# Performance work log

Measured on AMD Instinct MI355X. Metric: run time of the kernel, lower is better.

## Reference

```python
import jax, jax.numpy as jnp
import numpy as np

N_NODES, N_EDGES, N_REL, F_DIM, N_HEAD, N_LAYERS = 20000, 100000, 1000, 128, 4, 4
NEG_SLOPE = 0.2  # PyG GATv2Conv default negative_slope


def _gatv2_layer(x, ea_full, src, dst, Wl, bl, Wr, br, We, att, bias):
    # x: [N, F]; ea_full: [Etot, F] edge attrs (incl. self-loop rows)
    N = x.shape[0]
    H, C = att.shape  # heads, out-dim per head
    xl = (x @ Wl + bl).reshape(N, H, C)          # source-side projection
    xr = (x @ Wr + br).reshape(N, H, C)          # target-side projection
    ee = (ea_full @ We).reshape(-1, H, C)        # [Etot, H, C] edge embedding
    # GATv2 scoring: leaky_relu(x_i + x_j + e) . att
    e = jax.nn.leaky_relu(xl[src] + xr[dst] + ee, NEG_SLOPE)
    logits = jnp.einsum('ehc,hc->eh', e, att)    # [Etot, H]
    # segment softmax over edges grouped by destination node
    m = jax.ops.segment_max(logits, dst, num_segments=N)
    p = jnp.exp(logits - m[dst])
    denom = jax.ops.segment_sum(p, dst, num_segments=N)
    alpha = p / denom[dst]                       # [Etot, H]
    out = jax.ops.segment_sum(alpha[:, :, None] * xl[src], dst, num_segments=N)
    return out.mean(axis=1) + bias               # concat=False -> head mean


def setup_inputs() -> dict:
    key = jax.random.key(0)
    ks = jax.random.split(key, 12)
    N, E, R, F, H, L = N_NODES, N_EDGES, N_REL, F_DIM, N_HEAD, N_LAYERS
    HC = H * F
    s = 1.0 / np.sqrt(F)
    return {
        'x': jax.random.normal(ks[0], (N, F), jnp.float32),
        'edge_index': jax.random.randint(ks[1], (2, E), 0, N, dtype=jnp.int32),
        'relations': jax.random.normal(ks[2], (R, F), jnp.float32),
        'relation_index': jax.random.randint(ks[3], (E,), 0, R, dtype=jnp.int32),
        'Wl': jax.random.normal(ks[4], (L, F, HC), jnp.float32) * s,
        'bl': jnp.zeros((L, HC), jnp.float32),
        'Wr': jax.random.normal(ks[5], (L, F, HC), jnp.float32) * s,
        'br': jnp.zeros((L, HC), jnp.float32),
        'We': jax.random.normal(ks[6], (L, F, HC), jnp.float32) * s,
        'att': jax.random.normal(ks[7], (L, H, F), jnp.float32) * s,
        'bias': jnp.zeros((L, F), jnp.float32),
    }


def reference(x, edge_index, relations, relation_index, Wl, bl, Wr, br, We, att, bias):
    N = x.shape[0]
    sl = jnp.arange(N, dtype=edge_index.dtype)
    src = jnp.concatenate([edge_index[0], sl])   # add_self_loops=True
    dst = jnp.concatenate([edge_index[1], sl])
    ea = relations[relation_index]               # [E, F]
    # self-loop edge_attr uses fill_value='mean' (PyG default)
    ea_mean = ea.mean(axis=0)
    ea_full = jnp.concatenate([ea, jnp.broadcast_to(ea_mean, (N, ea.shape[1]))])
    h = x
    for l in range(N_LAYERS):
        h = _gatv2_layer(h, ea_full, src, dst, Wl[l], bl[l], Wr[l], br[l], We[l], att[l], bias[l])
    return (h, relations)
```

## Files before the change

kernel.cpp:

```cpp
#include <hip/hip_runtime.h>
#include <hip/hip_bf16.h>

#define N_NODES   20000
#define N_EDGES   100000
#define N_REL     1000
#define F_DIM     128
#define N_HEAD    4
#define HC        512
#define HC2       256
#define N_LAYERS  4
#define REL_EXT_ROWS 1008
#define NEG_SLOPE 0.2f
#define NODE_MB   ((N_NODES + 63) / 64)
#define REL_MB    ((REL_EXT_ROWS + 63) / 64)

typedef __attribute__((ext_vector_type(8))) short short8;
typedef __attribute__((ext_vector_type(4))) float floatx4;

__device__ __forceinline__ float loadIn(const void* p, size_t i, int f32) {
    if (f32) return ((const float*)p)[i];
    union { unsigned int u; float f; } c;
    c.u = ((unsigned int)((const unsigned short*)p)[i]) << 16;
    return c.f;
}

__device__ __forceinline__ unsigned short f2bf(float v) {
    __hip_bfloat16 b = __float2bfloat16(v);
    return *(unsigned short*)&b;
}

__device__ __forceinline__ void unpack2(unsigned int u, float& lo, float& hi) {
    union { unsigned int u; float f; } a, b;
    a.u = u << 16;
    b.u = u & 0xFFFF0000u;
    lo = a.f; hi = b.f;
}

__global__ void detect_kernel(const unsigned short* __restrict__ x, int* __restrict__ flag) {
    int t = threadIdx.x;
    int cnt = 0;
    for (int j = t; j < 256; j += 64) {
        int e = (x[j] >> 7) & 0xFF;
        if (e >= 143) cnt++;
    }
    for (int off = 32; off; off >>= 1) cnt += __shfl_xor(cnt, off);
    if (t == 0) flag[0] = (cnt >= 8) ? 1 : 0;
}


__global__ void hist_kernel(const int* __restrict__ dst, const int* __restrict__ rel,
                            int* __restrict__ deg, int* __restrict__ rcount) {
    int e = blockIdx.x * 256 + threadIdx.x;
    if (e < N_EDGES) {
        atomicAdd(&deg[dst[e]], 1);
        atomicAdd(&rcount[rel[e]], 1);
    }
}

__global__ void ea_mean_kernel(const int* __restrict__ rcount,
                               const void* __restrict__ relations,
                               float* __restrict__ ea_mean, const int* __restrict__ flag) {
    int f32 = flag[0];
    int b = blockIdx.x;
    int t = threadIdx.x;
    int col = t & 127;
    int rhalf = t >> 7;
    float acc = 0.f;
    for (int j = 0; j < 4; ++j) {
        int r = b * 8 + j * 2 + rhalf;
        acc += (float)rcount[r] * loadIn(relations, (size_t)r * F_DIM + col, f32);
    }
    __shared__ float part[256];
    part[t] = acc;
    __syncthreads();
    if (t < 128)
        atomicAdd(&ea_mean[col], (part[t] + part[t + 128]) * (1.f / (float)N_EDGES));
}

__global__ void relext_kernel(const void* __restrict__ relations,
                              const float* __restrict__ ea_mean,
                              unsigned short* __restrict__ rel_ext, const int* __restrict__ flag) {
    int idx = blockIdx.x * 256 + threadIdx.x;
    if (idx >= REL_EXT_ROWS * F_DIM) return;
    int f32 = flag[0];
    int r = idx >> 7;
    int c = idx & 127;
    float v;
    if (r < N_REL)       v = loadIn(relations, idx, f32);
    else if (r == N_REL) v = ea_mean[c];
    else                 v = 0.f;
    rel_ext[idx] = f2bf(v);
}

__global__ void scan_kernel(const int* __restrict__ deg,
                            int* __restrict__ row_start, int* __restrict__ cursor) {
    __shared__ int part[1024];
    int t = threadIdx.x;
    const int CH = (N_NODES + 1023) / 1024;
    int base = t * CH;
    int sum = 0;
    for (int j = 0; j < CH; ++j) {
        int idx = base + j;
        if (idx < N_NODES) sum += deg[idx];
    }
    part[t] = sum;
    __syncthreads();
    for (int off = 1; off < 1024; off <<= 1) {
        int u = (t >= off) ? part[t - off] : 0;
        __syncthreads();
        part[t] += u;
        __syncthreads();
    }
    int run = part[t] - sum;
    for (int j = 0; j < CH; ++j) {
        int idx = base + j;
        if (idx < N_NODES) {
            row_start[idx] = run;
            cursor[idx] = run;
            run += deg[idx];
        }
    }
    if (t == 1023) row_start[N_NODES] = part[1023];
}

__global__ void scatter_kernel(const int* __restrict__ src, const int* __restrict__ dst,
                               const int* __restrict__ rel, int* __restrict__ cursor,
                               int* __restrict__ csr_pack) {
    int e = blockIdx.x * 256 + threadIdx.x;
    if (e < N_EDGES) {
        int d = dst[e];
        int p = atomicAdd(&cursor[d], 1);
        csr_pack[p] = src[e] | (rel[e] << 16);
    }
}

__global__ void tail_kernel(const void* __restrict__ relations, void* __restrict__ out,
                            const int* __restrict__ flag) {
    int i = blockIdx.x * 256 + threadIdx.x;
    if (i >= N_REL * F_DIM) return;
    int f32 = flag[0];
    float v = loadIn(relations, i, f32);
    size_t o = (size_t)N_NODES * F_DIM + i;
    if (f32) ((float*)out)[o] = v;
    else     ((unsigned short*)out)[o] = f2bf(v);
}

__global__ void w_transpose_kernel(const void* __restrict__ Wl, const void* __restrict__ Wr,
                                   const void* __restrict__ We,
                                   unsigned short* __restrict__ Wt, const int* __restrict__ flag) {
    int f32 = flag[0];
    int k0 = blockIdx.x * 64;
    int n0 = blockIdx.y * 64;
    int mat = blockIdx.z;
    const void* src = (mat < 4) ? Wl : (mat < 8 ? Wr : We);
    size_t base = (size_t)(mat & 3) * F_DIM * HC;
    unsigned short* dst = Wt + (size_t)mat * HC * F_DIM;
    __shared__ float T[64][65];
    int t = threadIdx.x;
    int r = t >> 2, cq = t & 3;
    for (int j = 0; j < 16; ++j) {
        int n = cq * 16 + j;
        T[n][r] = loadIn(src, base + (size_t)(k0 + r) * HC + n0 + n, f32);
    }
    __syncthreads();
    for (int j = 0; j < 16; ++j) {
        int k = cq * 16 + j;
        dst[(size_t)(n0 + r) * F_DIM + k0 + k] = f2bf(T[r][k]);
    }
}

__launch_bounds__(256, 4)
__global__ void proj_kernel(const void* __restrict__ A_node, int a_input,
                            const unsigned short* __restrict__ rel_ext,
                            const unsigned short* __restrict__ Wlt,
                            const unsigned short* __restrict__ Wrt,
                            const unsigned short* __restrict__ Wet,
                            const void* __restrict__ bl, const void* __restrict__ br,
                            size_t boff,
                            unsigned short* __restrict__ xl,
                            unsigned short* __restrict__ xr,
                            unsigned short* __restrict__ re,
                            const int* __restrict__ flag) {
    __shared__ __align__(16) short As[64][136];
    __shared__ __align__(16) short BtRaw[128 * 72];
    int f32 = flag[0];
    int isNode = (blockIdx.x < NODE_MB);
    int m0 = (isNode ? blockIdx.x : (blockIdx.x - NODE_MB)) * 64;
    int M = isNode ? N_NODES : REL_EXT_ROWS;
    int tpb = isNode ? 2 : 1;
    int a_f32 = (isNode && a_input) ? f32 : 0;
    const void* A = isNode ? A_node : (const void*)rel_ext;
    int t = threadIdx.x;

    for (int j = 0; j < 4; ++j) {
        int c = t + j * 256;
        int row = c >> 4;
        int colc = (c & 15) * 8;
        int gm = m0 + row;
        short8 v = (short8){0, 0, 0, 0, 0, 0, 0, 0};
        if (gm < M) {
            size_t idx = (size_t)gm * F_DIM + colc;
            if (a_f32) {
                const float* Af = (const float*)A;
                for (int q = 0; q < 8; ++q) v[q] = (short)f2bf(Af[idx + q]);
            } else {
                v = *(const short8*)((const unsigned short*)A + idx);
            }
        }
        *(short8*)&As[row][colc] = v;
    }

    int wave = t >> 6, lane = t & 63;
    int wm = (wave >> 1) * 32, wn = (wave & 1) * 64;
    int r16 = lane & 15, quad = lane >> 4;

    for (int it = 0; it < tpb; ++it) {
        int nt = isNode ? (blockIdx.y * 2 + it) : blockIdx.y;
        const unsigned short* Wt = isNode ? ((nt < 4) ? Wlt : Wrt) : Wet;
        int n0 = (nt & 3) * 128;

        floatx4 acc[2][4];
        for (int mi = 0; mi < 2; ++mi)
            for (int ni = 0; ni < 4; ++ni)
                acc[mi][ni] = (floatx4){0.f, 0.f, 0.f, 0.f};

        for (int half = 0; half < 2; ++half) {
            __syncthreads();
            for (int j = 0; j < 4; ++j) {
                int c = t + j * 256;
                int nl = c >> 3;
                int kc = (c & 7) * 8;
                *(short8*)&BtRaw[nl * 72 + kc] =
                    *(const short8*)(Wt + (size_t)(n0 + nl) * F_DIM + half * 64 + kc);
            }
            __syncthreads();

            for (int kk = 0; kk < 2; ++kk) {
                short8 a[2], b[4];
                for (int mi = 0; mi < 2; ++mi)
                    a[mi] = *(const short8*)&As[wm + mi * 16 + r16][half * 64 + kk * 32 + quad * 8];
                for (int ni = 0; ni < 4; ++ni)
                    b[ni] = *(const short8*)&BtRaw[(wn + ni * 16 + r16) * 72 + kk * 32 + quad * 8];
                for (int mi = 0; mi < 2; ++mi)
                    for (int ni = 0; ni < 4; ++ni)
                        acc[mi][ni] = __builtin_amdgcn_mfma_f32_16x16x32_bf16(a[mi], b[ni], acc[mi][ni], 0, 0, 0);
            }
        }

        const void* bias = isNode ? ((nt < 4) ? bl : br) : nullptr;
        unsigned short* out = isNode ? ((nt < 4) ? xl : xr) : re;
        __syncthreads();
        for (int mi = 0; mi < 2; ++mi) {
            for (int ni = 0; ni < 4; ++ni) {
                int col = wn + ni * 16 + r16;
                float bv = bias ? loadIn(bias, boff + n0 + col, f32) : 0.f;
                for (int r = 0; r < 4; ++r) {
                    int rowl = wm + mi * 16 + quad * 4 + r;
                    BtRaw[rowl * 136 + col] = (short)f2bf(acc[mi][ni][r] + bv);
                }
            }
        }
        __syncthreads();
        for (int j = 0; j < 4; ++j) {
            int c = t + j * 256;
            int rowl = c >> 4;
            int colc = (c & 15) * 8;
            int gm = m0 + rowl;
            if (gm < M)
                *(short8*)(out + (size_t)gm * HC + n0 + colc) =
                    *(const short8*)&BtRaw[rowl * 136 + colc];
        }
    }
}

__launch_bounds__(256)
__global__ void edge_kernel(const uint4* __restrict__ xl4,
                            const uint4* __restrict__ xr4,
                            const uint4* __restrict__ re4,
                            const int* __restrict__ row_start,
                            const int* __restrict__ csr_pack,
                            const void* __restrict__ att, size_t att_off,
                            const void* __restrict__ bias, size_t bias_off,
                            void* __restrict__ hout, int final_layer,
                            const int* __restrict__ flag) {
    int f32 = flag[0];
    int w = threadIdx.x >> 6, lane = threadIdx.x & 63;
    int i = blockIdx.x * 4 + w;
    if (i >= N_NODES) return;

    float xrv[8], attv[8];
    {
        uint4 u = xr4[(size_t)i * 64 + lane];
        unpack2(u.x, xrv[0], xrv[1]); unpack2(u.y, xrv[2], xrv[3]);
        unpack2(u.z, xrv[4], xrv[5]); unpack2(u.w, xrv[6], xrv[7]);
        for (int q = 0; q < 8; ++q)
            attv[q] = loadIn(att, att_off + lane * 8 + q, f32);
    }

    float s = 0.f, acc[8];
    for (int q = 0; q < 8; ++q) acc[q] = 0.f;

    auto consume = [&](uint4 xu, uint4 ru) {
        float xv[8], rv[8];
        unpack2(xu.x, xv[0], xv[1]); unpack2(xu.y, xv[2], xv[3]);
        unpack2(xu.z, xv[4], xv[5]); unpack2(xu.w, xv[6], xv[7]);
        unpack2(ru.x, rv[0], rv[1]); unpack2(ru.y, rv[2], rv[3]);
        unpack2(ru.z, rv[4], rv[5]); unpack2(ru.w, rv[6], rv[7]);
        float part = 0.f;
        for (int q = 0; q < 8; ++q) {
            float t = xv[q] + xrv[q] + rv[q];
            t = fmaxf(t, NEG_SLOPE * t);
            part += t * attv[q];
        }
        for (int off = 8; off; off >>= 1) part += __shfl_xor(part, off);
        part = fminf(fmaxf(part, -60.f), 60.f);
        float p = __expf(part);
        s += p;
        for (int q = 0; q < 8; ++q) acc[q] += p * xv[q];
    };

    consume(xl4[(size_t)i * 64 + lane], re4[(size_t)N_REL * 64 + lane]);

    int e0 = row_start[i], e1 = row_start[i + 1];
    if (e0 < 0) e0 = 0;
    if (e1 > N_EDGES) e1 = N_EDGES;
    if (e1 < e0) e1 = e0;

    for (int b = e0; b < e1; b += 4) {
        int nb = e1 - b; if (nb > 4) nb = 4;
        uint4 xu[4], ru[4];
        #pragma unroll
        for (int k = 0; k < 4; ++k) {
            if (k < nb) {
                int pk = csr_pack[b + k];
                int sn = pk & 0xFFFF;        if (sn >= N_NODES) sn = 0;
                int rn = (pk >> 16) & 0x3FF; if (rn > N_REL) rn = N_REL;
                xu[k] = xl4[(size_t)sn * 64 + lane];
                ru[k] = re4[(size_t)rn * 64 + lane];
            }
        }
        #pragma unroll
        for (int k = 0; k < 4; ++k)
            if (k < nb) consume(xu[k], ru[k]);
    }

    float inv = 1.f / s;
    #pragma unroll
    for (int q = 0; q < 8; ++q) {
        float a = acc[q] * inv;
        a += __shfl_xor(a, 16);
        a += __shfl_xor(a, 32);
        acc[q] = a;
    }
    if (lane < 16) {
        if (final_layer && f32) {
            float* op = (float*)hout + (size_t)i * F_DIM + lane * 8;
            #pragma unroll
            for (int q = 0; q < 8; ++q)
                op[q] = acc[q] * 0.25f + loadIn(bias, bias_off + lane * 8 + q, f32);
        } else {
            unsigned short pkv[8];
            #pragma unroll
            for (int q = 0; q < 8; ++q)
                pkv[q] = f2bf(acc[q] * 0.25f + loadIn(bias, bias_off + lane * 8 + q, f32));
            *(short8*)((unsigned short*)hout + (size_t)i * F_DIM + lane * 8) = *(short8*)pkv;
        }
    }
}


extern "C" void kernel_launch(void* const* d_in, const int* in_sizes, int n_in,
                              void* d_out, int out_size, void* d_ws, size_t ws_size,
                              hipStream_t stream) {
    const void* x          = d_in[0];
    const int*  edge_index = (const int*)d_in[1];
    const void* relations  = d_in[2];
    const int*  rel_index  = (const int*)d_in[3];
    const void* Wl         = d_in[4];
    const void* bl         = d_in[5];
    const void* Wr         = d_in[6];
    const void* br         = d_in[7];
    const void* We         = d_in[8];
    const void* att        = d_in[9];
    const void* bias       = d_in[10];

    char* ws = (char*)d_ws;
    size_t off = 0;
    auto alloc = [&](size_t bytes) -> void* {
        void* p = ws + off;
        off = (off + bytes + 255) & ~(size_t)255;
        return p;
    };
    int*            flag     = (int*)alloc(4);
    int*            deg      = (int*)alloc(N_NODES * 4);
    int*            row_start= (int*)alloc((N_NODES + 1) * 4);
    int*            cursor   = (int*)alloc(N_NODES * 4);
    int*            rcount   = (int*)alloc(N_REL * 4);
    float*          ea_mean  = (float*)alloc(F_DIM * 4);
    int*            csr_pack = (int*)alloc(N_EDGES * 4);
    unsigned short* rel_ext  = (unsigned short*)alloc((size_t)REL_EXT_ROWS * F_DIM * 2);
    unsigned short* Wt       = (unsigned short*)alloc((size_t)12 * HC * F_DIM * 2);
    unsigned short* re       = (unsigned short*)alloc((size_t)REL_EXT_ROWS * HC * 2);
    unsigned short* hbuf     = (unsigned short*)alloc((size_t)N_NODES * F_DIM * 2);
    unsigned short* xl       = (unsigned short*)alloc((size_t)N_NODES * HC * 2);
    unsigned short* xr       = (unsigned short*)alloc((size_t)N_NODES * HC * 2);

    const int* esrc = edge_index;
    const int* edst = edge_index + N_EDGES;

    detect_kernel<<<1, 64, 0, stream>>>((const unsigned short*)x, flag);
    hipMemsetAsync(rcount, 0, N_REL * 4, stream);
    hipMemsetAsync(deg, 0, N_NODES * 4, stream);
    hipMemsetAsync(ea_mean, 0, F_DIM * 4, stream);
    hist_kernel<<<(N_EDGES + 255) / 256, 256, 0, stream>>>(edst, rel_index, deg, rcount);
    ea_mean_kernel<<<N_REL / 8, 256, 0, stream>>>(rcount, relations, ea_mean, flag);
    relext_kernel<<<(REL_EXT_ROWS * F_DIM + 255) / 256, 256, 0, stream>>>(relations, ea_mean, rel_ext, flag);
    scan_kernel<<<1, 1024, 0, stream>>>(deg, row_start, cursor);
    scatter_kernel<<<(N_EDGES + 255) / 256, 256, 0, stream>>>(esrc, edst, rel_index, cursor, csr_pack);
    w_transpose_kernel<<<dim3(2, 8, 12), 256, 0, stream>>>(Wl, Wr, We, Wt, flag);
    tail_kernel<<<(N_REL * F_DIM + 255) / 256, 256, 0, stream>>>(relations, d_out, flag);

    const void* hin = x;
    int a_input = 1;
    for (int l = 0; l < N_LAYERS; ++l) {
        const unsigned short* Wlt = Wt + (size_t)l * HC * F_DIM;
        const unsigned short* Wrt = Wt + (size_t)(4 + l) * HC * F_DIM;
        const unsigned short* Wet = Wt + (size_t)(8 + l) * HC * F_DIM;
        proj_kernel<<<dim3(NODE_MB + REL_MB, 4), 256, 0, stream>>>(
            hin, a_input, rel_ext, Wlt, Wrt, Wet,
            bl, br, (size_t)l * HC,
            xl, xr, re, flag);
        int final_layer = (l == N_LAYERS - 1);
        void* hout = final_layer ? d_out : (void*)hbuf;
        edge_kernel<<<(N_NODES + 3) / 4, 256, 0, stream>>>(
            (const uint4*)xl, (const uint4*)xr, (const uint4*)re,
            row_start, csr_pack,
            att, (size_t)l * N_HEAD * F_DIM,
            bias, (size_t)l * F_DIM,
            hout, final_layer, flag);
        hin = hbuf;
        a_input = 0;
    }
}
```

Before: 444.1 us.

## Software-pipeline edge gathers and read projection weights directly from global

```diff
diff --git a/kernel.cpp b/kernel.cpp
--- a/kernel.cpp
+++ b/kernel.cpp
@@ -182,7 +182,7 @@
                             unsigned short* __restrict__ re,
                             const int* __restrict__ flag) {
     __shared__ __align__(16) short As[64][136];
-    __shared__ __align__(16) short BtRaw[128 * 72];
+    __shared__ __align__(16) short Cs[64][136];
     int f32 = flag[0];
     int isNode = (blockIdx.x < NODE_MB);
     int m0 = (isNode ? blockIdx.x : (blockIdx.x - NODE_MB)) * 64;
@@ -213,6 +213,7 @@
     int wave = t >> 6, lane = t & 63;
     int wm = (wave >> 1) * 32, wn = (wave & 1) * 64;
     int r16 = lane & 15, quad = lane >> 4;
+    __syncthreads();
 
     for (int it = 0; it < tpb; ++it) {
         int nt = isNode ? (blockIdx.y * 2 + it) : blockIdx.y;
@@ -224,27 +225,17 @@
             for (int ni = 0; ni < 4; ++ni)
                 acc[mi][ni] = (floatx4){0.f, 0.f, 0.f, 0.f};
 
-        for (int half = 0; half < 2; ++half) {
-            __syncthreads();
-            for (int j = 0; j < 4; ++j) {
-                int c = t + j * 256;
-                int nl = c >> 3;
-                int kc = (c & 7) * 8;
-                *(short8*)&BtRaw[nl * 72 + kc] =
-                    *(const short8*)(Wt + (size_t)(n0 + nl) * F_DIM + half * 64 + kc);
-            }
-            __syncthreads();
-
-            for (int kk = 0; kk < 2; ++kk) {
-                short8 a[2], b[4];
-                for (int mi = 0; mi < 2; ++mi)
-                    a[mi] = *(const short8*)&As[wm + mi * 16 + r16][half * 64 + kk * 32 + quad * 8];
+        #pragma unroll
+        for (int ks = 0; ks < 4; ++ks) {
+            short8 a[2], b[4];
+            for (int mi = 0; mi < 2; ++mi)
+                a[mi] = *(const short8*)&As[wm + mi * 16 + r16][ks * 32 + quad * 8];
+            for (int ni = 0; ni < 4; ++ni)
+                b[ni] = *(const short8*)(Wt + (size_t)(n0 + wn + ni * 16 + r16) * F_DIM
+                                            + ks * 32 + quad * 8);
+            for (int mi = 0; mi < 2; ++mi)
                 for (int ni = 0; ni < 4; ++ni)
-                    b[ni] = *(const short8*)&BtRaw[(wn + ni * 16 + r16) * 72 + kk * 32 + quad * 8];
-                for (int mi = 0; mi < 2; ++mi)
-                    for (int ni = 0; ni < 4; ++ni)
-                        acc[mi][ni] = __builtin_amdgcn_mfma_f32_16x16x32_bf16(a[mi], b[ni], acc[mi][ni], 0, 0, 0);
-            }
+                    acc[mi][ni] = __builtin_amdgcn_mfma_f32_16x16x32_bf16(a[mi], b[ni], acc[mi][ni], 0, 0, 0);
         }
 
         const void* bias = isNode ? ((nt < 4) ? bl : br) : nullptr;
@@ -256,7 +247,7 @@
                 float bv = bias ? loadIn(bias, boff + n0 + col, f32) : 0.f;
                 for (int r = 0; r < 4; ++r) {
                     int rowl = wm + mi * 16 + quad * 4 + r;
-                    BtRaw[rowl * 136 + col] = (short)f2bf(acc[mi][ni][r] + bv);
+                    Cs[rowl][col] = (short)f2bf(acc[mi][ni][r] + bv);
                 }
             }
         }
@@ -268,7 +259,7 @@
             int gm = m0 + rowl;
             if (gm < M)
                 *(short8*)(out + (size_t)gm * HC + n0 + colc) =
-                    *(const short8*)&BtRaw[rowl * 136 + colc];
+                    *(const short8*)&Cs[rowl][colc];
         }
     }
 }
@@ -288,29 +279,48 @@
     int i = blockIdx.x * 4 + w;
     if (i >= N_NODES) return;
 
+    uint4 xru = xr4[(size_t)i * 64 + lane];
+    uint4 sxu = xl4[(size_t)i * 64 + lane];
+    uint4 sru = re4[(size_t)N_REL * 64 + lane];
+
+    int e0 = row_start[i], e1 = row_start[i + 1];
+    if (e0 < 0) e0 = 0;
+    if (e1 > N_EDGES) e1 = N_EDGES;
+    if (e1 < e0) e1 = e0;
+
+    uint4 xu[4], ru[4];
+    int nb = e1 - e0; if (nb > 4) nb = 4;
+    #pragma unroll
+    for (int k = 0; k < 4; ++k) {
+        if (k < nb) {
+            int pk = csr_pack[e0 + k];
+            int sn = pk & 0xFFFF;        if (sn >= N_NODES) sn = 0;
+            int rn = (pk >> 16) & 0x3FF; if (rn > N_REL) rn = N_REL;
+            xu[k] = xl4[(size_t)sn * 64 + lane];
+            ru[k] = re4[(size_t)rn * 64 + lane];
+        }
+    }
+
     float xrv[8], attv[8];
-    {
-        uint4 u = xr4[(size_t)i * 64 + lane];
-        unpack2(u.x, xrv[0], xrv[1]); unpack2(u.y, xrv[2], xrv[3]);
-        unpack2(u.z, xrv[4], xrv[5]); unpack2(u.w, xrv[6], xrv[7]);
-        for (int q = 0; q < 8; ++q)
-            attv[q] = loadIn(att, att_off + lane * 8 + q, f32);
-    }
+    unpack2(xru.x, xrv[0], xrv[1]); unpack2(xru.y, xrv[2], xrv[3]);
+    unpack2(xru.z, xrv[4], xrv[5]); unpack2(xru.w, xrv[6], xrv[7]);
+    for (int q = 0; q < 8; ++q)
+        attv[q] = loadIn(att, att_off + lane * 8 + q, f32);
 
     float s = 0.f, acc[8];
     for (int q = 0; q < 8; ++q) acc[q] = 0.f;
 
-    auto consume = [&](uint4 xu, uint4 ru) {
+    auto consume = [&](uint4 xuv, uint4 ruv) {
         float xv[8], rv[8];
-        unpack2(xu.x, xv[0], xv[1]); unpack2(xu.y, xv[2], xv[3]);
-        unpack2(xu.z, xv[4], xv[5]); unpack2(xu.w, xv[6], xv[7]);
-        unpack2(ru.x, rv[0], rv[1]); unpack2(ru.y, rv[2], rv[3]);
-        unpack2(ru.z, rv[4], rv[5]); unpack2(ru.w, rv[6], rv[7]);
+        unpack2(xuv.x, xv[0], xv[1]); unpack2(xuv.y, xv[2], xv[3]);
+        unpack2(xuv.z, xv[4], xv[5]); unpack2(xuv.w, xv[6], xv[7]);
+        unpack2(ruv.x, rv[0], rv[1]); unpack2(ruv.y, rv[2], rv[3]);
+        unpack2(ruv.z, rv[4], rv[5]); unpack2(ruv.w, rv[6], rv[7]);
         float part = 0.f;
         for (int q = 0; q < 8; ++q) {
-            float t = xv[q] + xrv[q] + rv[q];
-            t = fmaxf(t, NEG_SLOPE * t);
-            part += t * attv[q];
+            float tt = xv[q] + xrv[q] + rv[q];
+            tt = fmaxf(tt, NEG_SLOPE * tt);
+            part += tt * attv[q];
         }
         for (int off = 8; off; off >>= 1) part += __shfl_xor(part, off);
         part = fminf(fmaxf(part, -60.f), 60.f);
@@ -319,29 +329,29 @@
         for (int q = 0; q < 8; ++q) acc[q] += p * xv[q];
     };
 
-    consume(xl4[(size_t)i * 64 + lane], re4[(size_t)N_REL * 64 + lane]);
-
-    int e0 = row_start[i], e1 = row_start[i + 1];
-    if (e0 < 0) e0 = 0;
-    if (e1 > N_EDGES) e1 = N_EDGES;
-    if (e1 < e0) e1 = e0;
-
-    for (int b = e0; b < e1; b += 4) {
-        int nb = e1 - b; if (nb > 4) nb = 4;
-        uint4 xu[4], ru[4];
+    consume(sxu, sru);
+
+    int b = e0;
+    while (b < e1) {
+        int bn = b + 4;
+        int nbn = e1 - bn; if (nbn > 4) nbn = 4; if (nbn < 0) nbn = 0;
+        uint4 xun[4], run[4];
         #pragma unroll
         for (int k = 0; k < 4; ++k) {
-            if (k < nb) {
-                int pk = csr_pack[b + k];
+            if (k < nbn) {
+                int pk = csr_pack[bn + k];
                 int sn = pk & 0xFFFF;        if (sn >= N_NODES) sn = 0;
                 int rn = (pk >> 16) & 0x3FF; if (rn > N_REL) rn = N_REL;
-                xu[k] = xl4[(size_t)sn * 64 + lane];
-                ru[k] = re4[(size_t)rn * 64 + lane];
+                xun[k] = xl4[(size_t)sn * 64 + lane];
+                run[k] = re4[(size_t)rn * 64 + lane];
             }
         }
         #pragma unroll
         for (int k = 0; k < 4; ++k)
             if (k < nb) consume(xu[k], ru[k]);
+        #pragma unroll
+        for (int k = 0; k < 4; ++k) { xu[k] = xun[k]; ru[k] = run[k]; }
+        b = bn; nb = nbn;
     }
 
     float inv = 1.f / s;
```

New measurement: 529.0 us. 19.1% more time.
